# Performance work log

Hardware: AMD Instinct MI355X
Metric: run time of the kernel (lower is better)

Reference implementation:

```python
import jax, jax.numpy as jnp
import numpy as np

C = 192
NH = 8
DH = C // NH
WD, WH, WW = 6, 8, 8
SD, SH, SW = 3, 4, 4
B0, D, H, W = 1, 24, 64, 64  # divisible by window -> no padding
N = WD * WH * WW
EPS = 1e-5


def _layernorm(x, w, b):
    m = jnp.mean(x, axis=-1, keepdims=True)
    v = jnp.mean(jnp.square(x - m), axis=-1, keepdims=True)
    return (x - m) * jax.lax.rsqrt(v + EPS) * w + b


def _window_partition(x):
    # x: (B, Dp, Hp, Wp, C) -> (B*nW, N, C)
    B, Dp, Hp, Wp, Cc = x.shape
    x = x.reshape(B, Dp // WD, WD, Hp // WH, WH, Wp // WW, WW, Cc)
    x = x.transpose(0, 1, 3, 5, 2, 4, 6, 7)
    return x.reshape(-1, N, Cc)


def _window_reverse(win, B, Dp, Hp, Wp):
    Cc = win.shape[-1]
    x = win.reshape(B, Dp // WD, Hp // WH, Wp // WW, WD, WH, WW, Cc)
    x = x.transpose(0, 1, 4, 2, 5, 3, 6, 7)
    return x.reshape(B, Dp, Hp, Wp, Cc)


def _shift_attn_mask(Dp, Hp, Wp, dtype):
    # static numpy construction (Swin shifted-window mask)
    img = np.zeros((Dp, Hp, Wp), dtype=np.int32)
    cnt = 0
    d_sl = (slice(0, -WD), slice(-WD, -SD), slice(-SD, None))
    h_sl = (slice(0, -WH), slice(-WH, -SH), slice(-SH, None))
    w_sl = (slice(0, -WW), slice(-WW, -SW), slice(-SW, None))
    for ds in d_sl:
        for hs in h_sl:
            for ws in w_sl:
                img[ds, hs, ws] = cnt
                cnt += 1
    m = img.reshape(Dp // WD, WD, Hp // WH, WH, Wp // WW, WW)
    m = m.transpose(0, 2, 4, 1, 3, 5).reshape(-1, N)  # (nW, N)
    diff = m[:, None, :] - m[:, :, None]
    neg = np.finfo(np.float32).min
    mask = np.where(diff != 0, neg, 0.0).astype(np.float32)
    return jnp.asarray(mask, dtype=dtype)  # (nW, N, N)


def setup_inputs() -> dict:
    key = jax.random.key(0)
    ks = jax.random.split(key, 4)
    return {
        "q_map": jax.random.normal(ks[0], (B0, C, D, H, W), jnp.float32),
        "k_map": jax.random.normal(ks[1], (B0, C, D, H, W), jnp.float32),
        "v_map": jax.random.normal(ks[2], (B0, C, D, H, W), jnp.float32),
        "norm_q_w": jnp.ones((C,), jnp.float32),
        "norm_q_b": jnp.zeros((C,), jnp.float32),
        "norm_kv_w": jnp.ones((C,), jnp.float32),
        "norm_kv_b": jnp.zeros((C,), jnp.float32),
        "proj_w": jax.random.normal(ks[3], (C, C), jnp.float32) * 0.02,
        "proj_b": jnp.zeros((C,), jnp.float32),
    }


def reference(q_map, k_map, v_map, norm_q_w, norm_q_b, norm_kv_w, norm_kv_b, proj_w, proj_b):
    # (B,C,D,H,W) -> (B,D,H,W,C)
    q = q_map.transpose(0, 2, 3, 4, 1)
    k = k_map.transpose(0, 2, 3, 4, 1)
    v = v_map.transpose(0, 2, 3, 4, 1)
    # dims already divisible by window -> no pad
    Dp, Hp, Wp = D, H, W
    # cyclic shift
    q = jnp.roll(q, shift=(-SD, -SH, -SW), axis=(1, 2, 3))
    k = jnp.roll(k, shift=(-SD, -SH, -SW), axis=(1, 2, 3))
    v = jnp.roll(v, shift=(-SD, -SH, -SW), axis=(1, 2, 3))
    # window partition -> (Bwin, N, C)
    qw = _layernorm(_window_partition(q), norm_q_w, norm_q_b)
    kw = _layernorm(_window_partition(k), norm_kv_w, norm_kv_b)
    vw = _layernorm(_window_partition(v), norm_kv_w, norm_kv_b)
    Bwin = qw.shape[0]
    nW = Bwin // B0
    # heads
    qh = qw.reshape(Bwin, N, NH, DH).transpose(0, 2, 1, 3)
    kh = kw.reshape(Bwin, N, NH, DH).transpose(0, 2, 1, 3)
    vh = vw.reshape(Bwin, N, NH, DH).transpose(0, 2, 1, 3)
    scale = 1.0 / jnp.sqrt(jnp.asarray(DH, qh.dtype))
    scores = jnp.einsum('bhqd,bhkd->bhqk', qh, kh) * scale  # (Bwin,NH,N,N)
    mask = _shift_attn_mask(Dp, Hp, Wp, scores.dtype)  # (nW,N,N)
    scores = scores.reshape(B0, nW, NH, N, N) + mask[None, :, None]
    attn = jax.nn.softmax(scores, axis=-1).reshape(Bwin, NH, N, N)
    out = jnp.einsum('bhqk,bhkd->bhqd', attn, vh)
    out = out.transpose(0, 2, 1, 3).reshape(Bwin, N, C)
    out = jnp.einsum('bnc,oc->bno', out, proj_w) + proj_b
    out = _window_reverse(out, B0, Dp, Hp, Wp)
    out = jnp.roll(out, shift=(SD, SH, SW), axis=(1, 2, 3))
    return out.transpose(0, 4, 1, 2, 3)  # (B,C,D,H,W)
```

## Files before the change

kernel.cpp:

```cpp
#include <hip/hip_runtime.h>

typedef float f4v __attribute__((ext_vector_type(4)));
typedef _Float16 h8 __attribute__((ext_vector_type(8)));
typedef _Float16 h4 __attribute__((ext_vector_type(4)));
typedef _Float16 h2 __attribute__((ext_vector_type(2)));
typedef __fp16 f16x2 __attribute__((ext_vector_type(2)));


__device__ __forceinline__ float fast_exp2(float x) {
#if __has_builtin(__builtin_amdgcn_exp2f)
    return __builtin_amdgcn_exp2f(x);
#else
    return exp2f(x);
#endif
}
__device__ __forceinline__ float fast_rcp(float x) {
#if __has_builtin(__builtin_amdgcn_rcpf)
    return __builtin_amdgcn_rcpf(x);
#else
    return 1.0f / x;
#endif
}

__device__ __forceinline__ int region_slot(int n, int wi, int hi, int wj) {
    int s = 0;
    if (wi == 3 && (n >> 6) >= 3) s += 4;
    if (hi == 7 && ((n >> 3) & 7) >= 4) s += 2;
    if (wj == 7 && (n & 7) >= 4) s += 1;
    return s;
}

__global__ __launch_bounds__(256) void ln_stage_kernel(
    const float* __restrict__ q, const float* __restrict__ k, const float* __restrict__ v,
    const float* __restrict__ nqw, const float* __restrict__ nqb,
    const float* __restrict__ nkw, const float* __restrict__ nkb,
    _Float16* __restrict__ Qs, _Float16* __restrict__ Ks, _Float16* __restrict__ Vs)
{
    const int tid = threadIdx.x;
    const int bid = blockIdx.x;
    const int tensor = blockIdx.y;
    const int d = bid >> 5;
    const int h2 = bid & 31;

    const float* src = (tensor == 0) ? q : (tensor == 1) ? k : v;
    const float* gam = (tensor == 0) ? nqw : nkw;
    const float* bet = (tensor == 0) ? nqb : nkb;
    _Float16* dst = (tensor == 0) ? Qs : (tensor == 1) ? Ks : Vs;
    const float scale = (tensor == 0) ? (0.20412414523193154f * 1.44269504088896340f) : 1.0f;

    __shared__ __attribute__((aligned(16))) _Float16 tile[192][132];
    __shared__ __attribute__((aligned(16))) float psum4[4][128];
    __shared__ __attribute__((aligned(16))) float psq4[4][128];
    __shared__ float smean[128];
    __shared__ float srstd[128];
    __shared__ float sgam[192];
    __shared__ float sbet[192];

    if (tid < 192) { sgam[tid] = gam[tid]; sbet[tid] = bet[tid]; }

    const int lane = tid & 63;
    const int wid = tid >> 6;
    const int cg = tid >> 5;
    const int fp = tid & 31;

    {
        const float* base = src + (size_t)d * 4096 + (size_t)(h2 * 2) * 64 + fp * 4;
        f4v s4 = {}, ss4 = {};
        #pragma unroll
        for (int r = 0; r < 24; ++r) {
            const int c = r * 8 + cg;
            f4v x = *(const f4v*)(base + (size_t)c * 98304);
            s4 += x;
            ss4 += x * x;
            h4 hx;
            hx[0] = (_Float16)x[0]; hx[1] = (_Float16)x[1];
            hx[2] = (_Float16)x[2]; hx[3] = (_Float16)x[3];
            *(h4*)&tile[c][fp * 4] = hx;
        }
        #pragma unroll
        for (int m = 0; m < 4; ++m) {
            s4[m] += __shfl_xor(s4[m], 32);
            ss4[m] += __shfl_xor(ss4[m], 32);
        }
        if (lane < 32) {
            *(f4v*)&psum4[wid][lane * 4] = s4;
            *(f4v*)&psq4[wid][lane * 4] = ss4;
        }
    }
    __syncthreads();

    if (tid < 128) {
        float S = psum4[0][tid] + psum4[1][tid] + psum4[2][tid] + psum4[3][tid];
        float SS = psq4[0][tid] + psq4[1][tid] + psq4[2][tid] + psq4[3][tid];
        float mean = S * (1.0f / 192.0f);
        float var = SS * (1.0f / 192.0f) - mean * mean;
        smean[tid] = mean;
        srstd[tid] = rsqrtf(var + 1e-5f);
    }
    __syncthreads();

    {
        const int t = tid & 127;
        const int p = tid >> 7;
        const float mean = smean[t];
        const float rstd = srstd[t];
        const int h = h2 * 2 + (t >> 6);
        const int w = t & 63;
        int d_r = d + 21; if (d_r >= 24) d_r -= 24;
        int h_r = h + 60; if (h_r >= 64) h_r -= 64;
        int w_r = w + 60; if (w_r >= 64) w_r -= 64;
        const int wi = d_r / 6, td = d_r - wi * 6;
        const int hi = h_r >> 3, th = h_r & 7;
        const int wj = w_r >> 3, tw = w_r & 7;
        const int win = (wi * 8 + hi) * 8 + wj;
        const int n = (td * 8 + th) * 8 + tw;
        #pragma unroll
        for (int hh2 = 0; hh2 < 4; ++hh2) {
            const int head = p * 4 + hh2;
            _Float16* outp = dst + (size_t)(head * 256 + win) * 9216 + n * 24;
            #pragma unroll
            for (int cc = 0; cc < 3; ++cc) {
                const int c = head * 24 + cc * 8;
                h8 hv;
                #pragma unroll
                for (int j = 0; j < 8; ++j) {
                    float x = ((float)tile[c + j][t] - mean) * rstd * sgam[c + j] + sbet[c + j];
                    hv[j] = (_Float16)(x * scale);
                }
                *(h8*)(outp + cc * 8) = hv;
            }
        }
    }
}

__global__ __launch_bounds__(256) void wconv_kernel(const float* __restrict__ w,
                                                    _Float16* __restrict__ wb)
{
    int i = blockIdx.x * 256 + threadIdx.x;
    if (i < 192 * 192) wb[i] = (_Float16)w[i];
}

__device__ __forceinline__ void attn_epilogue(
    f4v o0, f4v o1, _Float16* __restrict__ Op,
    _Float16* __restrict__ AOw, int q0, int lane, int l15, int g)
{
    #pragma unroll
    for (int j = 0; j < 4; ++j) {
        float rs = __shfl(o1[j], (g << 4) | 8);
        float inv = fast_rcp(rs);
        const int r = 4 * g + j;
        Op[r * 24 + l15] = (_Float16)(o0[j] * inv);
        if (l15 < 8) Op[r * 24 + 16 + l15] = (_Float16)(o1[j] * inv);
    }
    asm volatile("s_waitcnt lgkmcnt(0)" ::: "memory");
    if (lane < 48) {
        h8 ov = *(const h8*)(Op + lane * 8);
        *(h8*)(AOw + (size_t)q0 * 24 + lane * 8) = ov;
    }
    asm volatile("" ::: "memory");
}

__global__ __launch_bounds__(512, 2) void attn_kernel(
    const _Float16* __restrict__ Qs, const _Float16* __restrict__ Ks,
    const _Float16* __restrict__ Vs, _Float16* __restrict__ AOs)
{
    const int win = blockIdx.x;
    const int head = blockIdx.y;
    const int tid = threadIdx.x;
    const int lane = tid & 63;
    const int wid = tid >> 6;
    const int l15 = lane & 15;
    const int g = lane >> 4;

    __shared__ __attribute__((aligned(16))) _Float16 Kh[384 * 36];
    __shared__ __attribute__((aligned(16))) _Float16 Vt[25 * 388];
    __shared__ __attribute__((aligned(16))) _Float16 Ob[8][2][16 * 24];

    const int wi = win >> 6, hi = (win >> 3) & 7, wj = win & 7;

    const size_t slab = (size_t)(head * 256 + win) * 9216;
    const _Float16* Kw = Ks + slab;
    const _Float16* Vw = Vs + slab;
    const _Float16* Qw = Qs + slab;
    _Float16* AOw = AOs + slab;

    const _Float16 mreg = (_Float16)6.32455532f;

    h8 qreg[3];
    #pragma unroll
    for (int qt = 0; qt < 3; ++qt) {
        h8 z = {};
        if (g < 3) {
            z = *(const h8*)(Qw + (size_t)(wid * 48 + qt * 16 + l15) * 24 + g * 8);
        } else {
            int slot = region_slot(wid * 48 + qt * 16 + l15, wi, hi, wj);
            #pragma unroll
            for (int j = 0; j < 8; ++j) z[j] = (slot == j) ? mreg : (_Float16)0.f;
        }
        qreg[qt] = z;
    }

    {
        const h8* K8 = (const h8*)Kw;
        const h8* V8 = (const h8*)Vw;
        #pragma unroll
        for (int it = 0; it < 5; ++it) {
            int idx = it * 512 + tid;
            if (idx < 1152) {
                int n = idx / 3;
                int ch = idx - n * 3;
                *(h8*)(Kh + n * 36 + ch * 8) = K8[idx];
            } else if (idx < 2304) {
                int i = idx - 1152;
                int n = i / 3;
                int ch = i - n * 3;
                h8 vv = V8[i];
                #pragma unroll
                for (int j = 0; j < 8; ++j) Vt[(ch * 8 + j) * 388 + n] = vv[j];
            }
        }
        if (tid < 384) {
            int slot = region_slot(tid, wi, hi, wj);
            h8 t;
            #pragma unroll
            for (int j = 0; j < 8; ++j) t[j] = (slot == j) ? mreg : (_Float16)0.f;
            *(h8*)(Kh + tid * 36 + 24) = t;
            Vt[24 * 388 + tid] = (_Float16)1.f;
        }
    }
    __syncthreads();

    const int v1row = (l15 < 8) ? (16 + l15) : 24;
    const int q0w = wid * 48;

    f4v o0_0 = {}, o1_0 = {}, o0_1 = {}, o1_1 = {};
    #pragma unroll
    for (int mt = 0; mt < 24; ++mt) {
        h8 kf = *(const h8*)(Kh + (16 * mt + l15) * 36 + g * 8);
        h4 v0 = *(const h4*)(Vt + l15 * 388 + 16 * mt + 4 * g);
        h4 v1 = *(const h4*)(Vt + v1row * 388 + 16 * mt + 4 * g);
        const f4v cinit = {-46.f, -46.f, -46.f, -46.f};

        {
            f4v s4 = __builtin_amdgcn_mfma_f32_16x16x32_f16(kf, qreg[0], cinit, 0, 0, 0);
            float p0 = fast_exp2(s4[0]), p1 = fast_exp2(s4[1]);
            float p2 = fast_exp2(s4[2]), p3 = fast_exp2(s4[3]);
            union { f16x2 gp[2]; h4 v; } pu;
            pu.gp[0] = __builtin_amdgcn_cvt_pkrtz(p0, p1);
            pu.gp[1] = __builtin_amdgcn_cvt_pkrtz(p2, p3);
            o0_0 = __builtin_amdgcn_mfma_f32_16x16x16f16(pu.v, v0, o0_0, 0, 0, 0);
            o1_0 = __builtin_amdgcn_mfma_f32_16x16x16f16(pu.v, v1, o1_0, 0, 0, 0);
        }
        {
            f4v s4 = __builtin_amdgcn_mfma_f32_16x16x32_f16(kf, qreg[1], cinit, 0, 0, 0);
            float p0 = fast_exp2(s4[0]), p1 = fast_exp2(s4[1]);
            float p2 = fast_exp2(s4[2]), p3 = fast_exp2(s4[3]);
            union { f16x2 gp[2]; h4 v; } pu;
            pu.gp[0] = __builtin_amdgcn_cvt_pkrtz(p0, p1);
            pu.gp[1] = __builtin_amdgcn_cvt_pkrtz(p2, p3);
            o0_1 = __builtin_amdgcn_mfma_f32_16x16x16f16(pu.v, v0, o0_1, 0, 0, 0);
            o1_1 = __builtin_amdgcn_mfma_f32_16x16x16f16(pu.v, v1, o1_1, 0, 0, 0);
        }
    }

    attn_epilogue(o0_0, o1_0, Ob[wid][0], AOw, q0w,      lane, l15, g);
    attn_epilogue(o0_1, o1_1, Ob[wid][1], AOw, q0w + 16, lane, l15, g);

    f4v o0a = {}, o0b = {}, o1a = {}, o1b = {};
    #pragma unroll
    for (int mt = 0; mt < 24; ++mt) {
        h8 kf = *(const h8*)(Kh + (16 * mt + l15) * 36 + g * 8);
        h4 v0 = *(const h4*)(Vt + l15 * 388 + 16 * mt + 4 * g);
        h4 v1 = *(const h4*)(Vt + v1row * 388 + 16 * mt + 4 * g);
        const f4v cinit = {-46.f, -46.f, -46.f, -46.f};
        f4v s4 = __builtin_amdgcn_mfma_f32_16x16x32_f16(kf, qreg[2], cinit, 0, 0, 0);
        float p0 = fast_exp2(s4[0]), p1 = fast_exp2(s4[1]);
        float p2 = fast_exp2(s4[2]), p3 = fast_exp2(s4[3]);
        union { f16x2 gp[2]; h4 v; } pu;
        pu.gp[0] = __builtin_amdgcn_cvt_pkrtz(p0, p1);
        pu.gp[1] = __builtin_amdgcn_cvt_pkrtz(p2, p3);
        if (mt & 1) {
            o0b = __builtin_amdgcn_mfma_f32_16x16x16f16(pu.v, v0, o0b, 0, 0, 0);
            o1b = __builtin_amdgcn_mfma_f32_16x16x16f16(pu.v, v1, o1b, 0, 0, 0);
        } else {
            o0a = __builtin_amdgcn_mfma_f32_16x16x16f16(pu.v, v0, o0a, 0, 0, 0);
            o1a = __builtin_amdgcn_mfma_f32_16x16x16f16(pu.v, v1, o1a, 0, 0, 0);
        }
    }
    attn_epilogue(o0a + o0b, o1a + o1b, Ob[wid][0], AOw, q0w + 32, lane, l15, g);
}

__global__ __launch_bounds__(256) void proj_kernel(
    const _Float16* __restrict__ AOs, const _Float16* __restrict__ Wb,
    const float* __restrict__ bias, _Float16* __restrict__ PO)
{
    const int bid = blockIdx.x;
    const int win = bid / 6;
    const int r6 = bid - win * 6;
    const int half = r6 / 3;
    const int mi = r6 - half * 3;
    const int tid = threadIdx.x;
    const int lane = tid & 63, wid = tid >> 6;
    const int l15 = lane & 15, g = lane >> 4;

    __shared__ __attribute__((aligned(16))) float tileT[4][192 * 17];
    float* Tw = tileT[wid];

    const int tb = half * 192 + mi * 64 + wid * 16;

    int hdk[6], sbk[6];
    #pragma unroll
    for (int kk = 0; kk < 6; ++kk) {
        int mm = kk * 4 + g;
        hdk[kk] = mm / 3;
        sbk[kk] = mm - 3 * hdk[kk];
    }

    h8 af[6];
    #pragma unroll
    for (int kk = 0; kk < 6; ++kk)
        af[kk] = *(const h8*)(AOs + (size_t)(hdk[kk] * 256 + win) * 9216
                                  + (size_t)(tb + l15) * 24 + sbk[kk] * 8);

    f4v acc[12];
    #pragma unroll
    for (int n = 0; n < 12; ++n) {
        f4v a = {};
        #pragma unroll
        for (int kk = 0; kk < 6; ++kk) {
            h8 bf = *(const h8*)(Wb + (size_t)(n * 16 + l15) * 192 + kk * 32 + g * 8);
            a = __builtin_amdgcn_mfma_f32_16x16x32_f16(af[kk], bf, a, 0, 0, 0);
        }
        acc[n] = a;
    }

    #pragma unroll
    for (int n = 0; n < 12; ++n) {
        float b = bias[n * 16 + l15];
        f4v vv = acc[n];
        vv[0] += b; vv[1] += b; vv[2] += b; vv[3] += b;
        *(f4v*)(Tw + (n * 16 + l15) * 17 + g * 4) = vv;
    }
    asm volatile("s_waitcnt lgkmcnt(0)" ::: "memory");

    _Float16* POw = PO + ((size_t)win * 384 + tb) * 192;
    #pragma unroll
    for (int b = 0; b < 6; ++b) {
        int flat = b * 64 + lane;
        int tl = flat / 24;
        int cc = (flat - tl * 24) * 8;
        h8 hv;
        #pragma unroll
        for (int m = 0; m < 8; ++m)
            hv[m] = (_Float16)Tw[(cc + m) * 17 + tl];
        *(h8*)(POw + (size_t)tl * 192 + cc) = hv;
    }
}

__global__ __launch_bounds__(256) void writeback_kernel(
    const _Float16* __restrict__ PO, float* __restrict__ out)
{
    const int bid = blockIdx.x;
    const int dd = bid >> 6;
    const int hh = bid & 63;
    const int tid = threadIdx.x;

    __shared__ __attribute__((aligned(16))) _Float16 Lw[64 * 196 + 8];

    int d_r = dd + 21; if (d_r >= 24) d_r -= 24;
    int h_r = hh + 60; if (h_r >= 64) h_r -= 64;
    const int wi = d_r / 6, td = d_r - wi * 6;
    const int hi = h_r >> 3, th = h_r & 7;
    const int winbase = (wi * 8 + hi) * 8;
    const int nbase = (td * 8 + th) * 8;

    #pragma unroll
    for (int it = 0; it < 6; ++it) {
        int idx = it * 256 + tid;
        int ww = idx / 24;
        int ch = idx - ww * 24;
        int w_r = ww + 60; if (w_r >= 64) w_r -= 64;
        int win = winbase + (w_r >> 3);
        int n = nbase + (w_r & 7);
        h8 v = *(const h8*)(PO + ((size_t)win * 384 + n) * 192 + ch * 8);
        *(h8*)(Lw + ww * 196 + ch * 8) = v;
    }
    __syncthreads();

    float* obase = out + (size_t)dd * 4096 + hh * 64;
    #pragma unroll
    for (int r = 0; r < 3; ++r) {
        const int c = r * 64 + (tid >> 2);
        float* orow = obase + (size_t)c * 98304;
        #pragma unroll
        for (int q = 0; q < 4; ++q) {
            const int w0 = q * 16 + (tid & 3) * 4;
            f4v v;
            #pragma unroll
            for (int m = 0; m < 4; ++m)
                v[m] = (float)Lw[(w0 + m) * 196 + c];
            *(f4v*)(orow + w0) = v;
        }
    }
}

extern "C" void kernel_launch(void* const* d_in, const int* in_sizes, int n_in,
                              void* d_out, int out_size, void* d_ws, size_t ws_size,
                              hipStream_t stream) {
    const float* q_map = (const float*)d_in[0];
    const float* k_map = (const float*)d_in[1];
    const float* v_map = (const float*)d_in[2];
    const float* nqw = (const float*)d_in[3];
    const float* nqb = (const float*)d_in[4];
    const float* nkw = (const float*)d_in[5];
    const float* nkb = (const float*)d_in[6];
    const float* pw = (const float*)d_in[7];
    const float* pb = (const float*)d_in[8];
    float* out = (float*)d_out;

    _Float16* ws = (_Float16*)d_ws;
    const size_t BUF = (size_t)8 * 256 * 384 * 24;
    _Float16* Qs = ws;
    _Float16* Ks = ws + BUF;
    _Float16* Vs = ws + 2 * BUF;
    _Float16* AOs = ws + 3 * BUF;
    _Float16* Wb = ws + 4 * BUF;
    _Float16* PO = Qs;

    ln_stage_kernel<<<dim3(768, 3), 256, 0, stream>>>(q_map, k_map, v_map,
                                                      nqw, nqb, nkw, nkb, Qs, Ks, Vs);
    wconv_kernel<<<144, 256, 0, stream>>>(pw, Wb);
    attn_kernel<<<dim3(256, 8), 512, 0, stream>>>(Qs, Ks, Vs, AOs);
    proj_kernel<<<1536, 256, 0, stream>>>(AOs, Wb, pb, PO);
    writeback_kernel<<<1536, 256, 0, stream>>>(PO, out);
}
```

Measured before the change: 208.2 us.

## Fuse output projection into writeback kernel, removing PO intermediate buffer

The projection GEMM and the un-shift/transposed writeback are merged into one kernel. Each block gathers its 64 output-row tokens from the attention output into shared memory, runs the MFMA projection, and writes fp32 results directly to the output in channel-major layout. This drops one kernel launch and the fp16 round trip through the PO buffer, in exchange for a row-gathered A-operand load and reuse of a shared-memory tile.

```diff
diff --git a/kernel.cpp b/kernel.cpp
--- a/kernel.cpp
+++ b/kernel.cpp
@@ -290,82 +290,20 @@
     attn_epilogue(o0a + o0b, o1a + o1b, Ob[wid][0], AOw, q0w + 32, lane, l15, g);
 }
 
-__global__ __launch_bounds__(256) void proj_kernel(
+__global__ __launch_bounds__(256) void proj_wb_kernel(
     const _Float16* __restrict__ AOs, const _Float16* __restrict__ Wb,
-    const float* __restrict__ bias, _Float16* __restrict__ PO)
-{
-    const int bid = blockIdx.x;
-    const int win = bid / 6;
-    const int r6 = bid - win * 6;
-    const int half = r6 / 3;
-    const int mi = r6 - half * 3;
-    const int tid = threadIdx.x;
-    const int lane = tid & 63, wid = tid >> 6;
-    const int l15 = lane & 15, g = lane >> 4;
-
-    __shared__ __attribute__((aligned(16))) float tileT[4][192 * 17];
-    float* Tw = tileT[wid];
-
-    const int tb = half * 192 + mi * 64 + wid * 16;
-
-    int hdk[6], sbk[6];
-    #pragma unroll
-    for (int kk = 0; kk < 6; ++kk) {
-        int mm = kk * 4 + g;
-        hdk[kk] = mm / 3;
-        sbk[kk] = mm - 3 * hdk[kk];
-    }
-
-    h8 af[6];
-    #pragma unroll
-    for (int kk = 0; kk < 6; ++kk)
-        af[kk] = *(const h8*)(AOs + (size_t)(hdk[kk] * 256 + win) * 9216
-                                  + (size_t)(tb + l15) * 24 + sbk[kk] * 8);
-
-    f4v acc[12];
-    #pragma unroll
-    for (int n = 0; n < 12; ++n) {
-        f4v a = {};
-        #pragma unroll
-        for (int kk = 0; kk < 6; ++kk) {
-            h8 bf = *(const h8*)(Wb + (size_t)(n * 16 + l15) * 192 + kk * 32 + g * 8);
-            a = __builtin_amdgcn_mfma_f32_16x16x32_f16(af[kk], bf, a, 0, 0, 0);
-        }
-        acc[n] = a;
-    }
-
-    #pragma unroll
-    for (int n = 0; n < 12; ++n) {
-        float b = bias[n * 16 + l15];
-        f4v vv = acc[n];
-        vv[0] += b; vv[1] += b; vv[2] += b; vv[3] += b;
-        *(f4v*)(Tw + (n * 16 + l15) * 17 + g * 4) = vv;
-    }
-    asm volatile("s_waitcnt lgkmcnt(0)" ::: "memory");
-
-    _Float16* POw = PO + ((size_t)win * 384 + tb) * 192;
-    #pragma unroll
-    for (int b = 0; b < 6; ++b) {
-        int flat = b * 64 + lane;
-        int tl = flat / 24;
-        int cc = (flat - tl * 24) * 8;
-        h8 hv;
-        #pragma unroll
-        for (int m = 0; m < 8; ++m)
-            hv[m] = (_Float16)Tw[(cc + m) * 17 + tl];
-        *(h8*)(POw + (size_t)tl * 192 + cc) = hv;
-    }
-}
-
-__global__ __launch_bounds__(256) void writeback_kernel(
-    const _Float16* __restrict__ PO, float* __restrict__ out)
+    const float* __restrict__ bias, float* __restrict__ out)
 {
     const int bid = blockIdx.x;
     const int dd = bid >> 6;
     const int hh = bid & 63;
     const int tid = threadIdx.x;
-
-    __shared__ __attribute__((aligned(16))) _Float16 Lw[64 * 196 + 8];
+    const int lane = tid & 63, wid = tid >> 6;
+    const int l15 = lane & 15, g = lane >> 4;
+
+    __shared__ __attribute__((aligned(16))) unsigned char lmem[192 * 68 * 4];
+    _Float16* Arows = (_Float16*)lmem;
+    float* tileT = (float*)lmem;
 
     int d_r = dd + 21; if (d_r >= 24) d_r -= 24;
     int h_r = hh + 60; if (h_r >= 64) h_r -= 64;
@@ -377,13 +315,42 @@
     #pragma unroll
     for (int it = 0; it < 6; ++it) {
         int idx = it * 256 + tid;
-        int ww = idx / 24;
-        int ch = idx - ww * 24;
-        int w_r = ww + 60; if (w_r >= 64) w_r -= 64;
+        int t = idx / 24;
+        int ch = idx - t * 24;
+        int w_r = t + 60; if (w_r >= 64) w_r -= 64;
         int win = winbase + (w_r >> 3);
         int n = nbase + (w_r & 7);
-        h8 v = *(const h8*)(PO + ((size_t)win * 384 + n) * 192 + ch * 8);
-        *(h8*)(Lw + ww * 196 + ch * 8) = v;
+        int head = ch / 3, sub = ch - 3 * head;
+        h8 v = *(const h8*)(AOs + (size_t)(head * 256 + win) * 9216
+                                + (size_t)n * 24 + sub * 8);
+        *(h8*)(Arows + t * 200 + ch * 8) = v;
+    }
+    __syncthreads();
+
+    h8 af[6];
+    #pragma unroll
+    for (int kk = 0; kk < 6; ++kk)
+        af[kk] = *(const h8*)(Arows + (wid * 16 + l15) * 200 + kk * 32 + g * 8);
+    __syncthreads();
+
+    f4v acc[12];
+    #pragma unroll
+    for (int n = 0; n < 12; ++n) {
+        f4v a = {};
+        #pragma unroll
+        for (int kk = 0; kk < 6; ++kk) {
+            h8 bf = *(const h8*)(Wb + (size_t)(n * 16 + l15) * 192 + kk * 32 + g * 8);
+            a = __builtin_amdgcn_mfma_f32_16x16x32_f16(af[kk], bf, a, 0, 0, 0);
+        }
+        acc[n] = a;
+    }
+
+    #pragma unroll
+    for (int n = 0; n < 12; ++n) {
+        float b = bias[n * 16 + l15];
+        f4v vv = acc[n];
+        vv[0] += b; vv[1] += b; vv[2] += b; vv[3] += b;
+        *(f4v*)(tileT + (n * 16 + l15) * 68 + wid * 16 + g * 4) = vv;
     }
     __syncthreads();
 
@@ -392,13 +359,11 @@
     for (int r = 0; r < 3; ++r) {
         const int c = r * 64 + (tid >> 2);
         float* orow = obase + (size_t)c * 98304;
+        const float* trow = tileT + c * 68;
         #pragma unroll
         for (int q = 0; q < 4; ++q) {
             const int w0 = q * 16 + (tid & 3) * 4;
-            f4v v;
-            #pragma unroll
-            for (int m = 0; m < 4; ++m)
-                v[m] = (float)Lw[(w0 + m) * 196 + c];
+            f4v v = *(const f4v*)(trow + w0);
             *(f4v*)(orow + w0) = v;
         }
     }
@@ -425,12 +390,10 @@
     _Float16* Vs = ws + 2 * BUF;
     _Float16* AOs = ws + 3 * BUF;
     _Float16* Wb = ws + 4 * BUF;
-    _Float16* PO = Qs;
 
     ln_stage_kernel<<<dim3(768, 3), 256, 0, stream>>>(q_map, k_map, v_map,
                                                       nqw, nqb, nkw, nkb, Qs, Ks, Vs);
     wconv_kernel<<<144, 256, 0, stream>>>(pw, Wb);
     attn_kernel<<<dim3(256, 8), 512, 0, stream>>>(Qs, Ks, Vs, AOs);
-    proj_kernel<<<1536, 256, 0, stream>>>(AOs, Wb, pb, PO);
-    writeback_kernel<<<1536, 256, 0, stream>>>(PO, out);
-}
+    proj_wb_kernel<<<1536, 256, 0, stream>>>(AOs, Wb, pb, out);
+}
```

After: 194.5 us. -6.6%, faster.
